# Kernel optimization log

Measured on AMD Instinct MI355X. Metric: run time of the kernel, lower is better.

## Reference

```python
import jax, jax.numpy as jnp
import numpy as np
import math

D_MODEL = 512
D_STATE = 16
D_CONV = 4
EXPAND = 2
D_INNER = EXPAND * D_MODEL          # 1024
D_HALF = D_INNER // 2               # 512
DT_RANK = math.ceil(D_MODEL / 16)   # 32
BATCH, SEQLEN = 2, 4096
DT_MIN, DT_MAX, DT_FLOOR = 0.001, 0.1, 1e-4


def setup_inputs() -> dict:
    key = jax.random.key(0)
    ks = jax.random.split(key, 9)

    def lin(k, fan_out, fan_in):
        return jax.random.normal(k, (fan_out, fan_in), jnp.float32) / np.float32(np.sqrt(fan_in))

    hidden_states = jax.random.normal(ks[0], (BATCH, SEQLEN, D_MODEL), jnp.float32)
    in_proj_w = lin(ks[1], D_INNER, D_MODEL)
    x_proj_w = lin(ks[2], DT_RANK + 2 * D_STATE, D_HALF)
    dt_std = np.float32(DT_RANK ** -0.5)
    dt_proj_w = jax.random.uniform(ks[3], (D_HALF, DT_RANK), jnp.float32, -dt_std, dt_std)
    dt = jnp.exp(jax.random.uniform(ks[4], (D_HALF,), jnp.float32)
                 * (math.log(DT_MAX) - math.log(DT_MIN)) + math.log(DT_MIN))
    dt = jnp.clip(dt, DT_FLOOR)
    dt_proj_b = dt + jnp.log(-jnp.expm1(-dt))  # inverse-softplus init
    A_log = jnp.log(jnp.tile(jnp.arange(1, D_STATE + 1, dtype=jnp.float32)[None, :], (D_HALF, 1)))
    D = jnp.ones((D_HALF,), jnp.float32)
    out_proj_w = lin(ks[5], D_MODEL, D_INNER)
    conv1d_x_w = jax.random.normal(ks[6], (D_HALF, 1, D_CONV), jnp.float32) / np.float32(np.sqrt(D_CONV))
    conv1d_z_w = jax.random.normal(ks[7], (D_HALF, 1, D_CONV), jnp.float32) / np.float32(np.sqrt(D_CONV))
    return dict(hidden_states=hidden_states, in_proj_w=in_proj_w,
                conv1d_x_w=conv1d_x_w, conv1d_z_w=conv1d_z_w,
                x_proj_w=x_proj_w, dt_proj_w=dt_proj_w, dt_proj_b=dt_proj_b,
                A_log=A_log, D=D, out_proj_w=out_proj_w)


def _dwconv_same(x, w):
    # x: (b, c, l); w: (c, 1, k) depthwise. torch padding='same' with k=4 pads (1, 2),
    # which matches lax 'SAME'.
    return jax.lax.conv_general_dilated(
        x, w, window_strides=(1,), padding='SAME',
        dimension_numbers=('NCH', 'OIH', 'NCH'),
        feature_group_count=x.shape[1])


def _selective_scan(x, delta, A, B, C, D):
    # x, delta: (b, d, l); A: (d, n); B, C: (b, n, l); D: (d,)
    dA = jnp.exp(jnp.einsum('bdl,dn->bldn', delta, A))        # (b, l, d, n)
    dBx = jnp.einsum('bdl,bnl,bdl->bldn', delta, B, x)        # (b, l, d, n)

    def combine(c1, c2):
        a1, b1 = c1
        a2, b2 = c2
        return a1 * a2, a2 * b1 + b2

    _, h = jax.lax.associative_scan(combine, (dA, dBx), axis=1)  # h: (b, l, d, n)
    y = jnp.einsum('bldn,bnl->bdl', h, C) + D[None, :, None] * x
    return y


def reference(hidden_states, in_proj_w, conv1d_x_w, conv1d_z_w, x_proj_w,
              dt_proj_w, dt_proj_b, A_log, D, out_proj_w):
    b, l, _ = hidden_states.shape
    xz = jnp.einsum('bld,ed->bel', hidden_states, in_proj_w)   # (b, d_inner, l)
    x, z = jnp.split(xz, 2, axis=1)                            # each (b, d_half, l)
    A = -jnp.exp(A_log.astype(jnp.float32))
    x = jax.nn.silu(_dwconv_same(x, conv1d_x_w))
    z = jax.nn.silu(_dwconv_same(z, conv1d_z_w))
    x_dbl = jnp.einsum('bdl,ed->bel', x, x_proj_w)             # (b, dt_rank+2n, l)
    dt_r = x_dbl[:, :DT_RANK]                                  # (b, dt_rank, l)
    Bm = x_dbl[:, DT_RANK:DT_RANK + D_STATE]                   # (b, n, l)
    Cm = x_dbl[:, DT_RANK + D_STATE:]                          # (b, n, l)
    dt = jnp.einsum('brl,dr->bdl', dt_r, dt_proj_w)            # (b, d_half, l)
    delta = jax.nn.softplus(dt + dt_proj_b.astype(jnp.float32)[None, :, None])
    y = _selective_scan(x, delta, A, Bm, Cm, D.astype(jnp.float32))
    y = jnp.concatenate([y, z], axis=1)                        # (b, d_inner, l)
    out = jnp.einsum('bdl,ed->ble', y, out_proj_w)             # (b, l, d_model)
    return out
```

## Files before the change

### kernel.cpp

```cpp
#include <hip/hip_runtime.h>
#include <math.h>

#define BB 2
#define LL 4096
#define DMODEL 512
#define DINNER 1024
#define DHALF 512
#define DSTATE 16
#define RK 32
#define NCH 64
#define NC 256
#define CLEN (LL/NC)
#define NG 16
#define GL (NC/NG)

typedef __attribute__((ext_vector_type(8))) short short8;
typedef __attribute__((ext_vector_type(4))) float f32x4;

__device__ __forceinline__ float silu_f(float v) { return v / (1.f + __expf(-v)); }

__device__ __forceinline__ unsigned short f2bf(float x) {
    unsigned int u = __float_as_uint(x);
    u += 0x7fffu + ((u >> 16) & 1u);
    return (unsigned short)(u >> 16);
}
__device__ __forceinline__ float bf2f(unsigned short u) {
    return __uint_as_float((unsigned int)u << 16);
}

__device__ __forceinline__ float softplus_f(float x) {
    return fmaxf(x, 0.f) + __logf(1.f + __expf(-fabsf(x)));
}

__device__ __forceinline__ void gload16(const unsigned short* g, unsigned short* l) {
    __builtin_amdgcn_global_load_lds((const __attribute__((address_space(1))) void*)g,
                                     (__attribute__((address_space(3))) void*)l, 16, 0, 0);
}

#define H4  1048576
#define W14 131072
#define W24 131072
#define W34 8192
__global__ void cast_all(const float* __restrict__ hid, const float* __restrict__ w1,
                         const float* __restrict__ w2, const float* __restrict__ w3,
                         unsigned short* __restrict__ Hb, unsigned short* __restrict__ Wb,
                         unsigned short* __restrict__ Wob, unsigned short* __restrict__ Wxb) {
    int i = blockIdx.x * 256 + threadIdx.x;
    const float* src; unsigned short* dst; int j;
    if (i < H4)                    { src = hid; dst = Hb;  j = i; }
    else if (i < H4 + W14)         { src = w1;  dst = Wb;  j = i - H4; }
    else if (i < H4 + W14 + W24)   { src = w2;  dst = Wob; j = i - H4 - W14; }
    else if (i < H4 + W14 + W24 + W34) { src = w3; dst = Wxb; j = i - H4 - W14 - W24; }
    else return;
    float4 v = *(const float4*)&src[(size_t)j * 4];
    ushort4 o = make_ushort4(f2bf(v.x), f2bf(v.y), f2bf(v.z), f2bf(v.w));
    *(ushort4*)&dst[(size_t)j * 4] = o;
}

template<int K, int E, bool BF16OUT>
__global__ __launch_bounds__(256) void gemm_mfma(const unsigned short* __restrict__ W,
                                                 const unsigned short* __restrict__ X,
                                                 void* __restrict__ outv) {
    __shared__ unsigned short Wa[128 * 64];
    __shared__ unsigned short Xa[128 * 64];
    const int tid = threadIdx.x;
    const int lane = tid & 63;
    const int w = tid >> 6;
    const int wr = w >> 1, wc = w & 1;
    const int frow = lane & 15;
    const int kg = lane >> 4;
    const int e0 = blockIdx.y * 128;
    const int r0 = blockIdx.x * 128;

    f32x4 acc[4][4] = {};

    for (int kt = 0; kt < K / 64; ++kt) {
        #pragma unroll
        for (int i = 0; i < 4; ++i) {
            int flat = i * 256 + tid;
            int row = flat >> 3;
            int slot = flat & 7;
            int chunk = slot ^ (row & 7);
            gload16(&W[(size_t)(e0 + row) * K + kt * 64 + chunk * 8], &Wa[flat * 8]);
            gload16(&X[(size_t)(r0 + row) * K + kt * 64 + chunk * 8], &Xa[flat * 8]);
        }
        __syncthreads();

        #pragma unroll
        for (int ks = 0; ks < 2; ++ks) {
            short8 af[4], bfr[4];
            #pragma unroll
            for (int m = 0; m < 4; ++m) {
                int row = wr * 64 + m * 16 + frow;
                int phys = (ks * 4 + kg) ^ (row & 7);
                af[m] = *(const short8*)&Wa[row * 64 + phys * 8];
            }
            #pragma unroll
            for (int n = 0; n < 4; ++n) {
                int row = wc * 64 + n * 16 + frow;
                int phys = (ks * 4 + kg) ^ (row & 7);
                bfr[n] = *(const short8*)&Xa[row * 64 + phys * 8];
            }
            #pragma unroll
            for (int m = 0; m < 4; ++m)
                #pragma unroll
                for (int n = 0; n < 4; ++n)
                    acc[m][n] = __builtin_amdgcn_mfma_f32_16x16x32_bf16(af[m], bfr[n], acc[m][n], 0, 0, 0);
        }
        __syncthreads();
    }

    #pragma unroll
    for (int m = 0; m < 4; ++m) {
        #pragma unroll
        for (int n = 0; n < 4; ++n) {
            int e = e0 + wr * 64 + m * 16 + kg * 4;
            int r = r0 + wc * 64 + n * 16 + frow;
            f32x4 a = acc[m][n];
            if constexpr (BF16OUT) {
                ushort4 o = make_ushort4(f2bf(a.x), f2bf(a.y), f2bf(a.z), f2bf(a.w));
                *(ushort4*)&((unsigned short*)outv)[(size_t)r * E + e] = o;
            } else {
                *(f32x4*)&((float*)outv)[(size_t)r * E + e] = a;
            }
        }
    }
}

__global__ __launch_bounds__(256) void gemm_xproj(const unsigned short* __restrict__ W,
                                                  const unsigned short* __restrict__ X,
                                                  float* __restrict__ out) {
    __shared__ unsigned short Xa[128 * 64];
    __shared__ unsigned short Wa[64 * 64];
    const int tid = threadIdx.x;
    const int lane = tid & 63;
    const int w = tid >> 6;
    const int frow = lane & 15;
    const int kg = lane >> 4;
    const int r0 = blockIdx.x * 128;

    f32x4 acc[4][2] = {};

    for (int kt = 0; kt < 512 / 64; ++kt) {
        #pragma unroll
        for (int i = 0; i < 4; ++i) {
            int flat = i * 256 + tid;
            int row = flat >> 3;
            int slot = flat & 7;
            int chunk = slot ^ (row & 7);
            gload16(&X[(size_t)(r0 + row) * 512 + kt * 64 + chunk * 8], &Xa[flat * 8]);
        }
        #pragma unroll
        for (int i = 0; i < 2; ++i) {
            int flat = i * 256 + tid;
            int row = flat >> 3;
            int slot = flat & 7;
            int chunk = slot ^ (row & 7);
            gload16(&W[(size_t)row * 512 + kt * 64 + chunk * 8], &Wa[flat * 8]);
        }
        __syncthreads();

        #pragma unroll
        for (int ks = 0; ks < 2; ++ks) {
            short8 af[4], bfr[2];
            #pragma unroll
            for (int m = 0; m < 4; ++m) {
                int row = m * 16 + frow;
                int phys = (ks * 4 + kg) ^ (row & 7);
                af[m] = *(const short8*)&Wa[row * 64 + phys * 8];
            }
            #pragma unroll
            for (int n = 0; n < 2; ++n) {
                int row = w * 32 + n * 16 + frow;
                int phys = (ks * 4 + kg) ^ (row & 7);
                bfr[n] = *(const short8*)&Xa[row * 64 + phys * 8];
            }
            #pragma unroll
            for (int m = 0; m < 4; ++m)
                #pragma unroll
                for (int n = 0; n < 2; ++n)
                    acc[m][n] = __builtin_amdgcn_mfma_f32_16x16x32_bf16(af[m], bfr[n], acc[m][n], 0, 0, 0);
        }
        __syncthreads();
    }

    #pragma unroll
    for (int m = 0; m < 4; ++m) {
        #pragma unroll
        for (int n = 0; n < 2; ++n) {
            int r = r0 + w * 32 + n * 16 + frow;
            int b = r >> 12;
            int l = r & (LL - 1);
            int e = m * 16 + kg * 4;
            #pragma unroll
            for (int i = 0; i < 4; ++i)
                out[((size_t)b * NCH + e + i) * LL + l] = acc[m][n][i];
        }
    }
}

__global__ void conv_silu(const unsigned short* __restrict__ xzb,
                          const float* __restrict__ wx, const float* __restrict__ wz,
                          float* __restrict__ xq, unsigned short* __restrict__ xqb,
                          unsigned short* __restrict__ ycb) {
    __shared__ float s[67][64];
    const int b = blockIdx.z;
    const int l0 = blockIdx.x * 64;
    const int c0 = blockIdx.y * 64;
    const int tid = threadIdx.x;
    for (int idx = tid; idx < 67 * 16; idx += 256) {
        int rr = idx >> 4, u = idx & 15;
        int l = l0 - 1 + rr;
        float4 f;
        if (l >= 0 && l < LL) {
            ushort4 v = *(const ushort4*)&xzb[((size_t)b * LL + l) * DINNER + c0 + u * 4];
            f = make_float4(bf2f(v.x), bf2f(v.y), bf2f(v.z), bf2f(v.w));
        } else f = make_float4(0.f, 0.f, 0.f, 0.f);
        *(float4*)&s[rr][u * 4] = f;
    }
    __syncthreads();
    const int cc = tid & 63;
    const int c = c0 + cc;
    const bool isx = (c < DHALF);
    const float* wp = isx ? &wx[c * 4] : &wz[(c - DHALF) * 4];
    float4 w = *(const float4*)wp;
    #pragma unroll
    for (int rep = 0; rep < 16; ++rep) {
        int ll = (tid >> 6) + rep * 4;
        float v = w.x * s[ll][cc] + w.y * s[ll + 1][cc] + w.z * s[ll + 2][cc] + w.w * s[ll + 3][cc];
        v = silu_f(v);
        int l = l0 + ll;
        if (isx) {
            xq[((size_t)b * LL + l) * DHALF + c] = v;
            xqb[((size_t)b * LL + l) * DHALF + c] = f2bf(v);
        } else {
            ycb[((size_t)b * LL + l) * DINNER + c] = f2bf(v);
        }
    }
}

__global__ __launch_bounds__(256) void scan1(const float* __restrict__ xq,
                      const float* __restrict__ xdbl, const float* __restrict__ A_log,
                      const float* __restrict__ dtw, const float* __restrict__ dtb,
                      float* __restrict__ pend, float* __restrict__ hend) {
    __shared__ float s[48][CLEN];
    const int b = blockIdx.z;
    const int d = blockIdx.y * 256 + threadIdx.x;
    const int c = blockIdx.x;
    const int tid = threadIdx.x;
    for (int idx = tid; idx < 48 * CLEN; idx += 256) {
        int ch = idx >> 4, ll = idx & (CLEN - 1);
        s[ch][ll] = xdbl[((size_t)b * NCH + ch) * LL + c * CLEN + ll];
    }
    float dtwreg[RK];
    #pragma unroll
    for (int r = 0; r < RK; r += 4) {
        float4 v = *(const float4*)&dtw[d * RK + r];
        dtwreg[r] = v.x; dtwreg[r+1] = v.y; dtwreg[r+2] = v.z; dtwreg[r+3] = v.w;
    }
    float Arow[DSTATE];
    #pragma unroll
    for (int n = 0; n < DSTATE; ++n) Arow[n] = -expf(A_log[d * DSTATE + n]);
    const float bias = dtb[d];
    float del[CLEN];
    #pragma unroll
    for (int t = 0; t < CLEN; ++t) del[t] = bias;
    __syncthreads();
    #pragma unroll
    for (int r = 0; r < RK; ++r) {
        float wv = dtwreg[r];
        #pragma unroll
        for (int q = 0; q < CLEN / 4; ++q) {
            float4 v = *(const float4*)&s[r][q * 4];
            del[q*4+0] = fmaf(v.x, wv, del[q*4+0]);
            del[q*4+1] = fmaf(v.y, wv, del[q*4+1]);
            del[q*4+2] = fmaf(v.z, wv, del[q*4+2]);
            del[q*4+3] = fmaf(v.w, wv, del[q*4+3]);
        }
    }
    #pragma unroll
    for (int t = 0; t < CLEN; ++t) del[t] = softplus_f(del[t]);

    float h[DSTATE], p[DSTATE];
    #pragma unroll
    for (int n = 0; n < DSTATE; ++n) { h[n] = 0.f; p[n] = 1.f; }
    #pragma unroll
    for (int t = 0; t < CLEN; ++t) {
        float dl = del[t];
        float xv = xq[((size_t)b * LL + c * CLEN + t) * DHALF + d];
        float dx = dl * xv;
        #pragma unroll
        for (int n = 0; n < DSTATE; ++n) {
            float dA = __expf(dl * Arow[n]);
            h[n] = fmaf(dA, h[n], dx * s[32 + n][t]);
            p[n] *= dA;
        }
    }
    size_t base = (((size_t)b * NC + c) * DSTATE) * DHALF + d;
    #pragma unroll
    for (int n = 0; n < DSTATE; ++n) {
        pend[base + (size_t)n * DHALF] = p[n];
        hend[base + (size_t)n * DHALF] = h[n];
    }
}

__global__ void scan2a(float* __restrict__ pend, float* __restrict__ hend,
                       float* __restrict__ gP, float* __restrict__ gH) {
    int flat = blockIdx.x * 256 + threadIdx.x;
    int d = flat & (DHALF - 1);
    int n = (flat >> 9) & (DSTATE - 1);
    int g = (flat >> 13) & (NG - 1);
    int b = flat >> 17;
    const size_t stride = (size_t)DSTATE * DHALF;
    size_t idx = (((size_t)b * NC + g * GL) * DSTATE + n) * DHALF + d;
    float P = 1.f, H = 0.f;
    #pragma unroll 4
    for (int j = 0; j < GL; ++j) {
        float p = pend[idx], h = hend[idx];
        pend[idx] = P; hend[idx] = H;
        H = fmaf(p, H, h);
        P *= p;
        idx += stride;
    }
    size_t gi = (((size_t)b * NG + g) * DSTATE + n) * DHALF + d;
    gP[gi] = P; gH[gi] = H;
}

__global__ void scan2b(const float* __restrict__ gP, float* __restrict__ gH) {
    int flat = blockIdx.x * 256 + threadIdx.x;
    int d = flat & (DHALF - 1);
    int n = (flat >> 9) & (DSTATE - 1);
    int b = flat >> 13;
    float h = 0.f;
    const size_t stride = (size_t)DSTATE * DHALF;
    size_t gi = (((size_t)b * NG) * DSTATE + n) * DHALF + d;
    for (int g = 0; g < NG; ++g) {
        float P = gP[gi], Hh = gH[gi];
        gH[gi] = h;
        h = fmaf(P, h, Hh);
        gi += stride;
    }
}

__global__ __launch_bounds__(256) void scan3(const float* __restrict__ xq,
                      const float* __restrict__ xdbl, const float* __restrict__ A_log,
                      const float* __restrict__ dtw, const float* __restrict__ dtb,
                      const float* __restrict__ Dp, const float* __restrict__ pend,
                      const float* __restrict__ hend, const float* __restrict__ gH,
                      unsigned short* __restrict__ ycb) {
    __shared__ float s[64][CLEN];
    const int b = blockIdx.z;
    const int d = blockIdx.y * 256 + threadIdx.x;
    const int c = blockIdx.x;
    const int tid = threadIdx.x;
    for (int idx = tid; idx < 64 * CLEN; idx += 256) {
        int ch = idx >> 4, ll = idx & (CLEN - 1);
        s[ch][ll] = xdbl[((size_t)b * NCH + ch) * LL + c * CLEN + ll];
    }
    float dtwreg[RK];
    #pragma unroll
    for (int r = 0; r < RK; r += 4) {
        float4 v = *(const float4*)&dtw[d * RK + r];
        dtwreg[r] = v.x; dtwreg[r+1] = v.y; dtwreg[r+2] = v.z; dtwreg[r+3] = v.w;
    }
    float Arow[DSTATE], h[DSTATE];
    size_t base = (((size_t)b * NC + c) * DSTATE) * DHALF + d;
    size_t gbase = (((size_t)b * NG + (c >> 4)) * DSTATE) * DHALF + d;
    #pragma unroll
    for (int n = 0; n < DSTATE; ++n) {
        Arow[n] = -expf(A_log[d * DSTATE + n]);
        h[n] = fmaf(pend[base + (size_t)n * DHALF], gH[gbase + (size_t)n * DHALF],
                    hend[base + (size_t)n * DHALF]);
    }
    const float bias = dtb[d];
    const float Dv = Dp[d];
    float del[CLEN];
    #pragma unroll
    for (int t = 0; t < CLEN; ++t) del[t] = bias;
    __syncthreads();
    #pragma unroll
    for (int r = 0; r < RK; ++r) {
        float wv = dtwreg[r];
        #pragma unroll
        for (int q = 0; q < CLEN / 4; ++q) {
            float4 v = *(const float4*)&s[r][q * 4];
            del[q*4+0] = fmaf(v.x, wv, del[q*4+0]);
            del[q*4+1] = fmaf(v.y, wv, del[q*4+1]);
            del[q*4+2] = fmaf(v.z, wv, del[q*4+2]);
            del[q*4+3] = fmaf(v.w, wv, del[q*4+3]);
        }
    }
    #pragma unroll
    for (int t = 0; t < CLEN; ++t) del[t] = softplus_f(del[t]);

    #pragma unroll
    for (int t = 0; t < CLEN; ++t) {
        float dl = del[t];
        float xv = xq[((size_t)b * LL + c * CLEN + t) * DHALF + d];
        float dx = dl * xv;
        float y = Dv * xv;
        #pragma unroll
        for (int n = 0; n < DSTATE; ++n) {
            float dA = __expf(dl * Arow[n]);
            h[n] = fmaf(dA, h[n], dx * s[32 + n][t]);
            y = fmaf(h[n], s[48 + n][t], y);
        }
        ycb[((size_t)b * LL + c * CLEN + t) * DINNER + d] = f2bf(y);
    }
}

extern "C" void kernel_launch(void* const* d_in, const int* in_sizes, int n_in,
                              void* d_out, int out_size, void* d_ws, size_t ws_size,
                              hipStream_t stream) {
    const float* hidden     = (const float*)d_in[0];
    const float* in_proj_w  = (const float*)d_in[1];
    const float* conv_x_w   = (const float*)d_in[2];
    const float* conv_z_w   = (const float*)d_in[3];
    const float* x_proj_w   = (const float*)d_in[4];
    const float* dt_proj_w  = (const float*)d_in[5];
    const float* dt_proj_b  = (const float*)d_in[6];
    const float* A_log      = (const float*)d_in[7];
    const float* Dp         = (const float*)d_in[8];
    const float* out_proj_w = (const float*)d_in[9];
    float* out = (float*)d_out;

    float* ws_f = (float*)d_ws;
    unsigned short* Wb  = (unsigned short*)(ws_f + 0);
    unsigned short* Wob = (unsigned short*)(ws_f + 262144);
    unsigned short* Wxb = (unsigned short*)(ws_f + 524288);
    unsigned short* xzb = (unsigned short*)(ws_f + 540672);
    float* xq   = ws_f + 4734976;
    unsigned short* xqb = (unsigned short*)(ws_f + 8929280);
    unsigned short* Hb  = (unsigned short*)(ws_f + 11026432);
    unsigned short* ycb = (unsigned short*)(ws_f + 13123584);
    float* xdbl = ws_f + 17317888;
    float* gP   = ws_f + 17842176;
    float* gH   = ws_f + 18104320;
    float* pend = (float*)xzb;
    float* hend = (float*)xqb;

    dim3 blk(256);

    cast_all<<<dim3((H4 + W14 + W24 + W34 + 255) / 256), blk, 0, stream>>>(
        hidden, in_proj_w, out_proj_w, x_proj_w, Hb, Wb, Wob, Wxb);
    gemm_mfma<DMODEL, DINNER, true><<<dim3(BB * LL / 128, DINNER / 128), blk, 0, stream>>>(Wb, Hb, xzb);
    conv_silu<<<dim3(LL / 64, DINNER / 64, BB), blk, 0, stream>>>(xzb, conv_x_w, conv_z_w, xq, xqb, ycb);
    gemm_xproj<<<dim3(BB * LL / 128), blk, 0, stream>>>(Wxb, xqb, xdbl);
    scan1<<<dim3(NC, DHALF / 256, BB), blk, 0, stream>>>(xq, xdbl, A_log, dt_proj_w, dt_proj_b, pend, hend);
    scan2a<<<dim3(BB * NG * DSTATE * DHALF / 256), blk, 0, stream>>>(pend, hend, gP, gH);
    scan2b<<<dim3(BB * DSTATE * DHALF / 256), blk, 0, stream>>>(gP, gH);
    scan3<<<dim3(NC, DHALF / 256, BB), blk, 0, stream>>>(xq, xdbl, A_log, dt_proj_w, dt_proj_b,
                                                         Dp, pend, hend, gH, ycb);
    gemm_mfma<DINNER, DMODEL, false><<<dim3(BB * LL / 128, DMODEL / 128), blk, 0, stream>>>(Wob, ycb, out);
}
```

Baseline: 148.9 us.

## Drop fp32 conv output, vectorize conv_silu, and halve scan chunk count

The fp32 copy of the conv/SiLU x output is removed, so scan1 and scan3 now read the bf16 buffer and convert it on load. This halves that tensor's write and read traffic and shrinks the workspace. conv_silu now has each thread handle four channels with float4 shared loads and ushort4 stores. The scan uses 128 chunks of length 32 instead of 256 of length 16, which cuts the chunk-state traffic and the scan2a work but doubles the serial length per thread and raises register pressure. It also feeds bf16-rounded x into the scan and the D skip term, which reduces numerical precision.

```diff
diff --git a/kernel.cpp b/kernel.cpp
--- a/kernel.cpp
+++ b/kernel.cpp
@@ -9,7 +9,7 @@
 #define DSTATE 16
 #define RK 32
 #define NCH 64
-#define NC 256
+#define NC 128
 #define CLEN (LL/NC)
 #define NG 16
 #define GL (NC/NG)
@@ -201,8 +201,7 @@
 
 __global__ void conv_silu(const unsigned short* __restrict__ xzb,
                           const float* __restrict__ wx, const float* __restrict__ wz,
-                          float* __restrict__ xq, unsigned short* __restrict__ xqb,
-                          unsigned short* __restrict__ ycb) {
+                          unsigned short* __restrict__ xqb, unsigned short* __restrict__ ycb) {
     __shared__ float s[67][64];
     const int b = blockIdx.z;
     const int l0 = blockIdx.x * 64;
@@ -219,27 +218,34 @@
         *(float4*)&s[rr][u * 4] = f;
     }
     __syncthreads();
-    const int cc = tid & 63;
-    const int c = c0 + cc;
+    const int ct = (tid & 15) * 4;
+    const int c = c0 + ct;
     const bool isx = (c < DHALF);
     const float* wp = isx ? &wx[c * 4] : &wz[(c - DHALF) * 4];
-    float4 w = *(const float4*)wp;
-    #pragma unroll
-    for (int rep = 0; rep < 16; ++rep) {
-        int ll = (tid >> 6) + rep * 4;
-        float v = w.x * s[ll][cc] + w.y * s[ll + 1][cc] + w.z * s[ll + 2][cc] + w.w * s[ll + 3][cc];
-        v = silu_f(v);
+    float4 w0 = *(const float4*)&wp[0];
+    float4 w1 = *(const float4*)&wp[4];
+    float4 w2 = *(const float4*)&wp[8];
+    float4 w3 = *(const float4*)&wp[12];
+    #pragma unroll
+    for (int rep = 0; rep < 4; ++rep) {
+        int ll = (tid >> 4) + rep * 16;
+        float4 t0 = *(const float4*)&s[ll][ct];
+        float4 t1 = *(const float4*)&s[ll + 1][ct];
+        float4 t2 = *(const float4*)&s[ll + 2][ct];
+        float4 t3 = *(const float4*)&s[ll + 3][ct];
+        float v0 = w0.x*t0.x + w0.y*t1.x + w0.z*t2.x + w0.w*t3.x;
+        float v1 = w1.x*t0.y + w1.y*t1.y + w1.z*t2.y + w1.w*t3.y;
+        float v2 = w2.x*t0.z + w2.y*t1.z + w2.z*t2.z + w2.w*t3.z;
+        float v3 = w3.x*t0.w + w3.y*t1.w + w3.z*t2.w + w3.w*t3.w;
+        ushort4 o = make_ushort4(f2bf(silu_f(v0)), f2bf(silu_f(v1)),
+                                 f2bf(silu_f(v2)), f2bf(silu_f(v3)));
         int l = l0 + ll;
-        if (isx) {
-            xq[((size_t)b * LL + l) * DHALF + c] = v;
-            xqb[((size_t)b * LL + l) * DHALF + c] = f2bf(v);
-        } else {
-            ycb[((size_t)b * LL + l) * DINNER + c] = f2bf(v);
-        }
-    }
-}
-
-__global__ __launch_bounds__(256) void scan1(const float* __restrict__ xq,
+        if (isx) *(ushort4*)&xqb[((size_t)b * LL + l) * DHALF + c] = o;
+        else     *(ushort4*)&ycb[((size_t)b * LL + l) * DINNER + c] = o;
+    }
+}
+
+__global__ __launch_bounds__(256) void scan1(const unsigned short* __restrict__ xqb,
                       const float* __restrict__ xdbl, const float* __restrict__ A_log,
                       const float* __restrict__ dtw, const float* __restrict__ dtb,
                       float* __restrict__ pend, float* __restrict__ hend) {
@@ -249,7 +255,7 @@
     const int c = blockIdx.x;
     const int tid = threadIdx.x;
     for (int idx = tid; idx < 48 * CLEN; idx += 256) {
-        int ch = idx >> 4, ll = idx & (CLEN - 1);
+        int ch = idx / CLEN, ll = idx % CLEN;
         s[ch][ll] = xdbl[((size_t)b * NCH + ch) * LL + c * CLEN + ll];
     }
     float dtwreg[RK];
@@ -287,7 +293,7 @@
     #pragma unroll
     for (int t = 0; t < CLEN; ++t) {
         float dl = del[t];
-        float xv = xq[((size_t)b * LL + c * CLEN + t) * DHALF + d];
+        float xv = bf2f(xqb[((size_t)b * LL + c * CLEN + t) * DHALF + d]);
         float dx = dl * xv;
         #pragma unroll
         for (int n = 0; n < DSTATE; ++n) {
@@ -314,7 +320,7 @@
     const size_t stride = (size_t)DSTATE * DHALF;
     size_t idx = (((size_t)b * NC + g * GL) * DSTATE + n) * DHALF + d;
     float P = 1.f, H = 0.f;
-    #pragma unroll 4
+    #pragma unroll
     for (int j = 0; j < GL; ++j) {
         float p = pend[idx], h = hend[idx];
         pend[idx] = P; hend[idx] = H;
@@ -342,7 +348,7 @@
     }
 }
 
-__global__ __launch_bounds__(256) void scan3(const float* __restrict__ xq,
+__global__ __launch_bounds__(256) void scan3(const unsigned short* __restrict__ xqb,
                       const float* __restrict__ xdbl, const float* __restrict__ A_log,
                       const float* __restrict__ dtw, const float* __restrict__ dtb,
                       const float* __restrict__ Dp, const float* __restrict__ pend,
@@ -354,7 +360,7 @@
     const int c = blockIdx.x;
     const int tid = threadIdx.x;
     for (int idx = tid; idx < 64 * CLEN; idx += 256) {
-        int ch = idx >> 4, ll = idx & (CLEN - 1);
+        int ch = idx / CLEN, ll = idx % CLEN;
         s[ch][ll] = xdbl[((size_t)b * NCH + ch) * LL + c * CLEN + ll];
     }
     float dtwreg[RK];
@@ -365,7 +371,7 @@
     }
     float Arow[DSTATE], h[DSTATE];
     size_t base = (((size_t)b * NC + c) * DSTATE) * DHALF + d;
-    size_t gbase = (((size_t)b * NG + (c >> 4)) * DSTATE) * DHALF + d;
+    size_t gbase = (((size_t)b * NG + (c / GL)) * DSTATE) * DHALF + d;
     #pragma unroll
     for (int n = 0; n < DSTATE; ++n) {
         Arow[n] = -expf(A_log[d * DSTATE + n]);
@@ -396,7 +402,7 @@
     #pragma unroll
     for (int t = 0; t < CLEN; ++t) {
         float dl = del[t];
-        float xv = xq[((size_t)b * LL + c * CLEN + t) * DHALF + d];
+        float xv = bf2f(xqb[((size_t)b * LL + c * CLEN + t) * DHALF + d]);
         float dx = dl * xv;
         float y = Dv * xv;
         #pragma unroll
@@ -428,28 +434,27 @@
     unsigned short* Wb  = (unsigned short*)(ws_f + 0);
     unsigned short* Wob = (unsigned short*)(ws_f + 262144);
     unsigned short* Wxb = (unsigned short*)(ws_f + 524288);
-    unsigned short* xzb = (unsigned short*)(ws_f + 540672);
-    float* xq   = ws_f + 4734976;
-    unsigned short* xqb = (unsigned short*)(ws_f + 8929280);
-    unsigned short* Hb  = (unsigned short*)(ws_f + 11026432);
-    unsigned short* ycb = (unsigned short*)(ws_f + 13123584);
-    float* xdbl = ws_f + 17317888;
-    float* gP   = ws_f + 17842176;
-    float* gH   = ws_f + 18104320;
-    float* pend = (float*)xzb;
-    float* hend = (float*)xqb;
+    unsigned short* Hb  = (unsigned short*)(ws_f + 540672);
+    unsigned short* xzb = (unsigned short*)(ws_f + 2637824);
+    unsigned short* xqb = (unsigned short*)(ws_f + 6832128);
+    unsigned short* ycb = (unsigned short*)(ws_f + 8929280);
+    float* xdbl = ws_f + 13123584;
+    float* gP   = ws_f + 13647872;
+    float* gH   = ws_f + 13910016;
+    float* pend = ws_f + 2637824;
+    float* hend = ws_f + 540672;
 
     dim3 blk(256);
 
     cast_all<<<dim3((H4 + W14 + W24 + W34 + 255) / 256), blk, 0, stream>>>(
         hidden, in_proj_w, out_proj_w, x_proj_w, Hb, Wb, Wob, Wxb);
     gemm_mfma<DMODEL, DINNER, true><<<dim3(BB * LL / 128, DINNER / 128), blk, 0, stream>>>(Wb, Hb, xzb);
-    conv_silu<<<dim3(LL / 64, DINNER / 64, BB), blk, 0, stream>>>(xzb, conv_x_w, conv_z_w, xq, xqb, ycb);
+    conv_silu<<<dim3(LL / 64, DINNER / 64, BB), blk, 0, stream>>>(xzb, conv_x_w, conv_z_w, xqb, ycb);
     gemm_xproj<<<dim3(BB * LL / 128), blk, 0, stream>>>(Wxb, xqb, xdbl);
-    scan1<<<dim3(NC, DHALF / 256, BB), blk, 0, stream>>>(xq, xdbl, A_log, dt_proj_w, dt_proj_b, pend, hend);
+    scan1<<<dim3(NC, DHALF / 256, BB), blk, 0, stream>>>(xqb, xdbl, A_log, dt_proj_w, dt_proj_b, pend, hend);
     scan2a<<<dim3(BB * NG * DSTATE * DHALF / 256), blk, 0, stream>>>(pend, hend, gP, gH);
     scan2b<<<dim3(BB * DSTATE * DHALF / 256), blk, 0, stream>>>(gP, gH);
-    scan3<<<dim3(NC, DHALF / 256, BB), blk, 0, stream>>>(xq, xdbl, A_log, dt_proj_w, dt_proj_b,
+    scan3<<<dim3(NC, DHALF / 256, BB), blk, 0, stream>>>(xqb, xdbl, A_log, dt_proj_w, dt_proj_b,
                                                          Dp, pend, hend, gH, ycb);
     gemm_mfma<DINNER, DMODEL, false><<<dim3(BB * LL / 128, DMODEL / 128), blk, 0, stream>>>(Wob, ycb, out);
 }
```

Measured after the change: 134.8 us. 9.5% less time.
